# Kernel tuning notes

Measured on AMD Instinct MI355X. Metric: run time of the kernel, lower is better.

## Reference

```python
import jax, jax.numpy as jnp
from jax import lax
import numpy as np


def setup_inputs() -> dict:
    key = jax.random.key(0)
    encode_image = jax.random.normal(key, (32, 3, 512, 512), dtype=jnp.float32)
    return {"encode_image": encode_image, "w": 5}


def _box_blur(x, w):
    # cv2.blur with ksize (w, w): normalized box filter, BORDER_REFLECT_101 padding.
    # Implemented as a separable depthwise convolution (two 1D average passes).
    B, C, H, W = x.shape
    p = w // 2  # w is odd -> symmetric padding, matches cv2 default anchor
    xp = jnp.pad(x, ((0, 0), (0, 0), (p, p), (p, p)), mode="reflect")  # REFLECT_101
    kh = jnp.full((C, 1, w, 1), 1.0 / w, dtype=x.dtype)  # vertical pass
    kw = jnp.full((C, 1, 1, w), 1.0 / w, dtype=x.dtype)  # horizontal pass
    dn = ("NCHW", "OIHW", "NCHW")
    y = lax.conv_general_dilated(xp, kh, (1, 1), "VALID",
                                 dimension_numbers=dn, feature_group_count=C)
    y = lax.conv_general_dilated(y, kw, (1, 1), "VALID",
                                 dimension_numbers=dn, feature_group_count=C)
    return y  # (B, C, H, W)


def reference(encode_image, w):
    # Faithful to Smooth.forward: replaces noise_and_cover[0] with the box-blurred
    # image; we return the blurred tensor (the only modified element).
    return _box_blur(encode_image, w)
```

## Files before the change

kernel.cpp:

```cpp
#include <hip/hip_runtime.h>


#define TILE 64
#define HALO 2
#define TIN  (TILE + 2 * HALO)
#define PADI (TIN + 1)

__global__ __launch_bounds__(256) void smooth_box5_kernel(
    const float* __restrict__ in, float* __restrict__ out, int H, int W)
{
    __shared__ float s_in[TIN][PADI];
    __shared__ float s_h [TIN][TILE];

    const int tid   = threadIdx.x;
    const int tileX = blockIdx.x * TILE;
    const int tileY = blockIdx.y * TILE;
    const long long plane = blockIdx.z;

    const float* __restrict__ ip = in  + plane * (long long)H * W;
    float*       __restrict__ op = out + plane * (long long)H * W;

    #pragma unroll 4
    for (int i = tid; i < TIN * TIN; i += 256) {
        int r = i / TIN;
        int c = i - r * TIN;
        int gy = tileY + r - HALO;
        int gx = tileX + c - HALO;
        gy = (gy < 0) ? -gy : ((gy >= H) ? (2 * H - 2 - gy) : gy);
        gx = (gx < 0) ? -gx : ((gx >= W) ? (2 * W - 2 - gx) : gx);
        s_in[r][c] = ip[(long long)gy * W + gx];
    }
    __syncthreads();

    #pragma unroll 4
    for (int i = tid; i < TIN * TILE; i += 256) {
        int r = i >> 6;
        int c = i & (TILE - 1);
        float v = s_in[r][c] + s_in[r][c + 1] + s_in[r][c + 2]
                + s_in[r][c + 3] + s_in[r][c + 4];
        s_h[r][c] = v * 0.2f;
    }
    __syncthreads();

    #pragma unroll 4
    for (int i = tid; i < TILE * TILE; i += 256) {
        int r = i >> 6;
        int c = i & (TILE - 1);
        float v = s_h[r][c] + s_h[r + 1][c] + s_h[r + 2][c]
                + s_h[r + 3][c] + s_h[r + 4][c];
        op[(long long)(tileY + r) * W + (tileX + c)] = v * 0.2f;
    }
}

extern "C" void kernel_launch(void* const* d_in, const int* in_sizes, int n_in,
                              void* d_out, int out_size, void* d_ws, size_t ws_size,
                              hipStream_t stream) {
    const float* img = (const float*)d_in[0];
    float* out = (float*)d_out;
    const int B = 32, C = 3, H = 512, W = 512;
    dim3 grid(W / TILE, H / TILE, B * C);
    dim3 block(256);
    smooth_box5_kernel<<<grid, block, 0, stream>>>(img, out, H, W);
}
```

Baseline: 192.5 us.

## Replace shared-memory tiled blur with register sliding-window row strips

Drops the LDS two-pass tiling. Each thread now owns four adjacent columns of a 32-row strip and computes the horizontal 5-tap sums from float4/float2 global loads. A running vertical sum over a six-row register ring buffer replaces the vertical pass. This removes shared-memory traffic and barriers and vectorises loads and stores, at the cost of redundant neighbour loads across threads and fewer threads per block.

```diff
diff --git a/kernel.cpp b/kernel.cpp
--- a/kernel.cpp
+++ b/kernel.cpp
@@ -1,54 +1,81 @@
 #include <hip/hip_runtime.h>
 
 
-#define TILE 64
-#define HALO 2
-#define TIN  (TILE + 2 * HALO)
-#define PADI (TIN + 1)
+#define IMG_H 512
+#define IMG_W 512
+#define NF4   (IMG_W / 4)
+#define STRIP 32
+#define NSTRIPS (IMG_H / STRIP)
 
-__global__ __launch_bounds__(256) void smooth_box5_kernel(
-    const float* __restrict__ in, float* __restrict__ out, int H, int W)
+struct F4 { float x, y, z, w; };
+
+__global__ __launch_bounds__(128) void smooth_box5_reg(
+    const float* __restrict__ in, float* __restrict__ out)
 {
-    __shared__ float s_in[TIN][PADI];
-    __shared__ float s_h [TIN][TILE];
+    const int c4 = threadIdx.x;
+    const int r0 = blockIdx.x * STRIP;
+    const size_t planeOff = (size_t)blockIdx.y * (IMG_H * IMG_W);
+    const float* __restrict__ ip = in + planeOff;
+    float*       __restrict__ op = out + planeOff;
+    const int xb = c4 * 4;
 
-    const int tid   = threadIdx.x;
-    const int tileX = blockIdx.x * TILE;
-    const int tileY = blockIdx.y * TILE;
-    const long long plane = blockIdx.z;
+    auto hrow = [&](int r) -> F4 {
+        int ry = (r < 0) ? -r : r;
+        ry = (ry >= IMG_H) ? (2 * IMG_H - 2 - ry) : ry;
+        const float* row = ip + (size_t)ry * IMG_W;
+        const float4 b = *(const float4*)(row + xb);
+        float a2, a3, cc0, cc1;
+        if (c4 > 0) {
+            const float2 a = *(const float2*)(row + xb - 2);
+            a2 = a.x; a3 = a.y;
+        } else {
+            a2 = b.z; a3 = b.y;
+        }
+        if (c4 < NF4 - 1) {
+            const float2 c = *(const float2*)(row + xb + 4);
+            cc0 = c.x; cc1 = c.y;
+        } else {
+            cc0 = b.z; cc1 = b.y;
+        }
+        const float s = b.x + b.y + b.z + b.w;
+        F4 h;
+        h.x = s - b.w + a2 + a3;
+        h.y = s + a3;
+        h.z = s + cc0;
+        h.w = s - b.x + cc0 + cc1;
+        return h;
+    };
 
-    const float* __restrict__ ip = in  + plane * (long long)H * W;
-    float*       __restrict__ op = out + plane * (long long)H * W;
+    F4 h[6];
+    h[0] = hrow(r0 - 2);
+    h[1] = hrow(r0 - 1);
+    h[2] = hrow(r0);
+    h[3] = hrow(r0 + 1);
+    h[4] = hrow(r0 + 2);
+    F4 S;
+    S.x = h[0].x + h[1].x + h[2].x + h[3].x + h[4].x;
+    S.y = h[0].y + h[1].y + h[2].y + h[3].y + h[4].y;
+    S.z = h[0].z + h[1].z + h[2].z + h[3].z + h[4].z;
+    S.w = h[0].w + h[1].w + h[2].w + h[3].w + h[4].w;
 
-    #pragma unroll 4
-    for (int i = tid; i < TIN * TIN; i += 256) {
-        int r = i / TIN;
-        int c = i - r * TIN;
-        int gy = tileY + r - HALO;
-        int gx = tileX + c - HALO;
-        gy = (gy < 0) ? -gy : ((gy >= H) ? (2 * H - 2 - gy) : gy);
-        gx = (gx < 0) ? -gx : ((gx >= W) ? (2 * W - 2 - gx) : gx);
-        s_in[r][c] = ip[(long long)gy * W + gx];
-    }
-    __syncthreads();
+    const float inv = 0.2f * 0.2f;
+    float* orow = op + (size_t)r0 * IMG_W + xb;
 
-    #pragma unroll 4
-    for (int i = tid; i < TIN * TILE; i += 256) {
-        int r = i >> 6;
-        int c = i & (TILE - 1);
-        float v = s_in[r][c] + s_in[r][c + 1] + s_in[r][c + 2]
-                + s_in[r][c + 3] + s_in[r][c + 4];
-        s_h[r][c] = v * 0.2f;
-    }
-    __syncthreads();
-
-    #pragma unroll 4
-    for (int i = tid; i < TILE * TILE; i += 256) {
-        int r = i >> 6;
-        int c = i & (TILE - 1);
-        float v = s_h[r][c] + s_h[r + 1][c] + s_h[r + 2][c]
-                + s_h[r + 3][c] + s_h[r + 4][c];
-        op[(long long)(tileY + r) * W + (tileX + c)] = v * 0.2f;
+    #pragma unroll
+    for (int rr = 0; rr < STRIP; ++rr) {
+        float4 o;
+        o.x = S.x * inv; o.y = S.y * inv; o.z = S.z * inv; o.w = S.w * inv;
+        *(float4*)orow = o;
+        orow += IMG_W;
+        if (rr < STRIP - 1) {
+            const int inew = (rr + 5) % 6;
+            const int iold = rr % 6;
+            h[inew] = hrow(r0 + rr + 3);
+            S.x += h[inew].x - h[iold].x;
+            S.y += h[inew].y - h[iold].y;
+            S.z += h[inew].z - h[iold].z;
+            S.w += h[inew].w - h[iold].w;
+        }
     }
 }
 
@@ -57,8 +84,8 @@
                               hipStream_t stream) {
     const float* img = (const float*)d_in[0];
     float* out = (float*)d_out;
-    const int B = 32, C = 3, H = 512, W = 512;
-    dim3 grid(W / TILE, H / TILE, B * C);
-    dim3 block(256);
-    smooth_box5_kernel<<<grid, block, 0, stream>>>(img, out, H, W);
+    const int BC = 32 * 3;
+    dim3 grid(NSTRIPS, BC);
+    dim3 block(128);
+    smooth_box5_reg<<<grid, block, 0, stream>>>(img, out);
 }
```

After: 204.8 us. +6.4%, slower.
